# Performance work log

Hardware: AMD Instinct MI355X
Metric: run time of the kernel (lower is better)

The kernel has to match this reference:

```python
import jax, jax.numpy as jnp
import numpy as np

N = 20000
M = 32          # max_neighbors
IN_DIM = 256
OUT_DIM = 256
H = 4           # num_heads
D = OUT_DIM // H  # head_dim = 64
LN_EPS = 1e-5
NEG_INF = -1.0e9


def setup_inputs() -> dict:
    key = jax.random.key(0)
    ks = jax.random.split(key, 6)
    h = jax.random.normal(ks[0], (N, IN_DIM), dtype=jnp.float32)
    neighbor_idx = jax.random.randint(ks[1], (N, M), 0, N, dtype=jnp.int32)
    neighbor_mask = jax.random.randint(ks[2], (N, M), 0, 2, dtype=jnp.int32)
    # parameters (xavier-ish scaling)
    W = jax.random.normal(ks[3], (IN_DIM, OUT_DIM), dtype=jnp.float32) / np.sqrt(IN_DIM)
    a_l = jax.random.normal(ks[4], (H, D), dtype=jnp.float32) / np.sqrt(D)
    a_r = jax.random.normal(ks[5], (H, D), dtype=jnp.float32) / np.sqrt(D)
    ln_gamma = jnp.ones((OUT_DIM,), dtype=jnp.float32)
    ln_beta = jnp.zeros((OUT_DIM,), dtype=jnp.float32)
    return {"h": h, "neighbor_idx": neighbor_idx, "neighbor_mask": neighbor_mask,
            "W": W, "a_l": a_l, "a_r": a_r, "ln_gamma": ln_gamma, "ln_beta": ln_beta}


def reference(h, neighbor_idx, neighbor_mask, W, a_l, a_r, ln_gamma, ln_beta):
    h_proj = h @ W                                   # [N, OUT_DIM]
    h_heads = h_proj.reshape(N, H, D)                # [N, H, D]
    # per-node score halves; gathering scalars instead of full features for er
    el = jnp.einsum('nhd,hd->nh', h_heads, a_l)      # [N, H]
    er_node = jnp.einsum('nhd,hd->nh', h_heads, a_r) # [N, H]
    er = er_node[neighbor_idx]                       # [N, M, H]
    e = jax.nn.leaky_relu(el[:, None, :] + er, negative_slope=0.2)  # [N, M, H]
    e = jnp.where(neighbor_mask[:, :, None] == 0, NEG_INF, e)
    alpha = jax.nn.softmax(e, axis=1)                # softmax over neighbors
    neigh_h = h_heads[neighbor_idx]                  # [N, M, H, D]
    out_heads = jnp.einsum('nmh,nmhd->nhd', alpha, neigh_h)
    H_cat = out_heads.reshape(N, OUT_DIM)
    res = h_proj                                     # in_dim == out_dim -> res_proj is None
    out = jax.nn.gelu(H_cat + res, approximate=False)
    # LayerNorm over last dim
    mu = jnp.mean(out, axis=-1, keepdims=True)
    var = jnp.var(out, axis=-1, keepdims=True)
    out = (out - mu) * jax.lax.rsqrt(var + LN_EPS) * ln_gamma + ln_beta
    return out
```

## Files before the change

kernel.cpp:

```cpp
#include <hip/hip_runtime.h>
#include <math.h>

#define N_NODES 20000
#define M_NEI   32
#define DIM     256
#define H_HEADS 4
#define D_HEAD  64
#define LN_EPS  1e-5f
#define NEG_INF -1.0e9f
#define APAD    264

using short8  = __attribute__((ext_vector_type(8))) short;
using short4v = __attribute__((ext_vector_type(4))) short;
using floatx4 = __attribute__((ext_vector_type(4))) float;
using floatx2 = __attribute__((ext_vector_type(2))) float;
using uintx4  = __attribute__((ext_vector_type(4))) unsigned int;

__device__ __forceinline__ float bf2f(unsigned short u) {
    union { unsigned int i; float f; } c; c.i = ((unsigned int)u) << 16; return c.f;
}
__device__ __forceinline__ float u2f(unsigned int i) {
    union { unsigned int i; float f; } c; c.i = i; return c.f;
}
__device__ __forceinline__ unsigned short f2bf(float f) {
    union { float f; unsigned int i; } c; c.f = f;
    unsigned int x = c.i;
    x += 0x7fffu + ((x >> 16) & 1u);
    return (unsigned short)(x >> 16);
}
__device__ __forceinline__ bool in_is_fp32(const void* gamma) {
    return *(const unsigned int*)gamma == 0x3F800000u;
}

__global__ void k_prep(const void* __restrict__ W, const void* __restrict__ gamma,
                       unsigned short* __restrict__ Wt) {
    const bool f32 = in_is_fp32(gamma);
    const int n = blockIdx.x;
    const int k = threadIdx.x;
    float w = f32 ? ((const float*)W)[(size_t)k * DIM + n]
                  : bf2f(((const unsigned short*)W)[(size_t)k * DIM + n]);
    Wt[(size_t)n * DIM + k] = f2bf(w);
}

__global__ __launch_bounds__(256) void k_gemm(const void* __restrict__ A,
                                              const void* __restrict__ gamma,
                                              const unsigned short* __restrict__ Bt,
                                              const void* __restrict__ al,
                                              const void* __restrict__ ar,
                                              unsigned short* __restrict__ hp_h,
                                              float* __restrict__ el_h,
                                              float* __restrict__ er_h) {
    __shared__ unsigned short sA[32][APAD];
    const bool f32 = in_is_fp32(gamma);
    const int t    = threadIdx.x;
    const int m0   = blockIdx.x * 32;

    #pragma unroll
    for (int it = 0; it < 4; ++it) {
        int chunk = it * 256 + t;
        int row   = chunk >> 5;
        int c16   = chunk & 31;
        short8 v;
        if (!f32) {
            v = *(const short8*)((const unsigned short*)A + (size_t)(m0 + row) * DIM + c16 * 8);
        } else {
            const float* ap = (const float*)A + (size_t)(m0 + row) * DIM + c16 * 8;
            #pragma unroll
            for (int j = 0; j < 8; ++j) v[j] = (short)f2bf(ap[j]);
        }
        *(short8*)&sA[row][c16 * 8] = v;
    }
    __syncthreads();

    const int hd   = t >> 6;
    const int lane = t & 63;
    const int r    = lane & 15;
    const int quad = lane >> 4;
    const int n0   = hd * 64;

    floatx4 acc[2][4];
    #pragma unroll
    for (int rf = 0; rf < 2; ++rf)
        #pragma unroll
        for (int c = 0; c < 4; ++c) acc[rf][c] = (floatx4){0.f, 0.f, 0.f, 0.f};

    #pragma unroll
    for (int k0 = 0; k0 < DIM; k0 += 32) {
        short8 a0 = *(const short8*)&sA[r][k0 + quad * 8];
        short8 a1 = *(const short8*)&sA[16 + r][k0 + quad * 8];
        #pragma unroll
        for (int c = 0; c < 4; ++c) {
            short8 b = *(const short8*)(Bt + (size_t)(n0 + c * 16 + r) * DIM + k0 + quad * 8);
            acc[0][c] = __builtin_amdgcn_mfma_f32_16x16x32_bf16(a0, b, acc[0][c], 0, 0, 0);
            acc[1][c] = __builtin_amdgcn_mfma_f32_16x16x32_bf16(a1, b, acc[1][c], 0, 0, 0);
        }
    }

    float alv[4], arv[4];
    #pragma unroll
    for (int c = 0; c < 4; ++c) {
        int col = n0 + c * 16 + r;
        if (f32) { alv[c] = ((const float*)al)[col]; arv[c] = ((const float*)ar)[col]; }
        else     { alv[c] = bf2f(((const unsigned short*)al)[col]);
                   arv[c] = bf2f(((const unsigned short*)ar)[col]); }
    }

    #pragma unroll
    for (int rf = 0; rf < 2; ++rf) {
        #pragma unroll
        for (int rr = 0; rr < 4; ++rr) {
            const int row = m0 + rf * 16 + quad * 4 + rr;
            float sl = 0.f, sr = 0.f;
            #pragma unroll
            for (int c = 0; c < 4; ++c) {
                float v = acc[rf][c][rr];
                sl += v * alv[c];
                sr += v * arv[c];
                hp_h[((size_t)hd * N_NODES + row) * D_HEAD + c * 16 + r] = f2bf(v);
            }
            #pragma unroll
            for (int off = 1; off < 16; off <<= 1) {
                sl += __shfl_xor(sl, off);
                sr += __shfl_xor(sr, off);
            }
            if (r == 0) {
                el_h[(size_t)hd * N_NODES + row] = sl;
                er_h[(size_t)hd * N_NODES + row] = sr;
            }
        }
    }
}

__global__ __launch_bounds__(256) void k_attn_h(const int* __restrict__ nidx,
                                                const int* __restrict__ nmask,
                                                const unsigned short* __restrict__ hp_h,
                                                const float* __restrict__ el_h,
                                                const float* __restrict__ er_h,
                                                unsigned short* __restrict__ out_h) {
    __shared__ int2 s_oa[32][33];

    const int hd  = blockIdx.x & 3;
    const int nb0 = (blockIdx.x >> 2) * 32;
    const int t   = threadIdx.x;

    {
        const int m   = t & 31;
        const int sub = t >> 5;
        #pragma unroll
        for (int it = 0; it < 4; ++it) {
            const int nl  = it * 8 + sub;
            const int n   = nb0 + nl;
            const int idx = nidx[(size_t)n * M_NEI + m];
            const int msk = nmask[(size_t)n * M_NEI + m];
            float e = el_h[(size_t)hd * N_NODES + n] + er_h[(size_t)hd * N_NODES + idx];
            e = (e > 0.f) ? e : 0.2f * e;
            e = msk ? e : NEG_INF;
            float mx = e;
            #pragma unroll
            for (int off = 1; off < 32; off <<= 1) mx = fmaxf(mx, __shfl_xor(mx, off, 32));
            float a = expf(e - mx);
            float sm = a;
            #pragma unroll
            for (int off = 1; off < 32; off <<= 1) sm += __shfl_xor(sm, off, 32);
            int2 oa;
            oa.x = idx * (D_HEAD * 2);
            union { float f; int i; } c; c.f = a / sm;
            oa.y = c.i;
            s_oa[nl][m] = oa;
        }
    }
    __syncthreads();

    const int wave = t >> 6;
    const int lane = t & 63;
    const int g    = lane >> 3;
    const int s    = lane & 7;
    const int nl   = wave * 8 + g;
    const int n    = nb0 + nl;
    const char* tbl = (const char*)hp_h + (size_t)hd * N_NODES * (D_HEAD * 2) + s * 16;

    floatx2 acc[4];
    #pragma unroll
    for (int j = 0; j < 4; ++j) acc[j] = (floatx2){0.f, 0.f};

    #pragma unroll
    for (int m = 0; m < M_NEI; ++m) {
        const int2  oa = s_oa[nl][m];
        const float aa = u2f((unsigned int)oa.y);
        uintx4 u = *(const uintx4*)(tbl + oa.x);
        #pragma unroll
        for (int j = 0; j < 4; ++j) {
            floatx2 f = { u2f(u[j] << 16), u2f(u[j] & 0xffff0000u) };
            acc[j] += (floatx2){aa, aa} * f;
        }
    }

    {
        uintx4 u = *(const uintx4*)((const char*)hp_h
                     + ((size_t)hd * N_NODES + n) * (D_HEAD * 2) + s * 16);
        #pragma unroll
        for (int j = 0; j < 4; ++j) {
            floatx2 f = { u2f(u[j] << 16), u2f(u[j] & 0xffff0000u) };
            acc[j] += f;
        }
    }

    short8 o;
    #pragma unroll
    for (int j = 0; j < 4; ++j) {
        o[2 * j]     = (short)f2bf(acc[j][0]);
        o[2 * j + 1] = (short)f2bf(acc[j][1]);
    }
    *(short8*)(out_h + ((size_t)hd * N_NODES + n) * D_HEAD + s * 8) = o;
}

__global__ __launch_bounds__(256) void k_final(const unsigned short* __restrict__ out_h,
                                               const void* __restrict__ gamma,
                                               const void* __restrict__ beta,
                                               void* __restrict__ out) {
    const bool f32 = in_is_fp32(gamma);
    const int wave = threadIdx.x >> 6;
    const int lane = threadIdx.x & 63;
    const int n    = blockIdx.x * 4 + wave;
    const int h    = lane >> 4;
    const int d0   = (lane & 15) * 4;

    const size_t off = ((size_t)h * N_NODES + n) * D_HEAD + d0;
    short4v ov = *(const short4v*)(out_h + off);

    float x[4], s1 = 0.f, s2 = 0.f;
    #pragma unroll
    for (int i = 0; i < 4; ++i) {
        float xi = bf2f((unsigned short)ov[i]);
        xi = 0.5f * xi * (1.f + erff(xi * 0.70710678118654752f));
        x[i] = xi;
        s1 += xi;
        s2 += xi * xi;
    }
    #pragma unroll
    for (int offv = 1; offv < 64; offv <<= 1) {
        s1 += __shfl_xor(s1, offv);
        s2 += __shfl_xor(s2, offv);
    }
    const float mu  = s1 * (1.f / 256.f);
    float var = s2 * (1.f / 256.f) - mu * mu;
    var = fmaxf(var, 0.f);
    const float inv = rsqrtf(var + LN_EPS);

    if (f32) {
        const float* gp = (const float*)gamma + lane * 4;
        const float* bp = (const float*)beta  + lane * 4;
        float* op = (float*)out + (size_t)n * DIM + lane * 4;
        #pragma unroll
        for (int i = 0; i < 4; ++i)
            op[i] = (x[i] - mu) * inv * gp[i] + bp[i];
    } else {
        const unsigned short* gp = (const unsigned short*)gamma + lane * 4;
        const unsigned short* bp = (const unsigned short*)beta  + lane * 4;
        short4v o;
        #pragma unroll
        for (int i = 0; i < 4; ++i) {
            float y = (x[i] - mu) * inv * bf2f(gp[i]) + bf2f(bp[i]);
            o[i] = (short)f2bf(y);
        }
        *(short4v*)((unsigned short*)out + (size_t)n * DIM + lane * 4) = o;
    }
}

extern "C" void kernel_launch(void* const* d_in, const int* in_sizes, int n_in,
                              void* d_out, int out_size, void* d_ws, size_t ws_size,
                              hipStream_t stream) {
    const void* h     = d_in[0];
    const int*  nidx  = (const int*)d_in[1];
    const int*  nmask = (const int*)d_in[2];
    const void* W     = d_in[3];
    const void* al    = d_in[4];
    const void* ar    = d_in[5];
    const void* gamma = d_in[6];
    const void* beta  = d_in[7];

    unsigned short* Wt    = (unsigned short*)d_ws;
    unsigned short* hp_h  = (unsigned short*)((char*)d_ws + 131072);
    unsigned short* out_h = (unsigned short*)((char*)d_ws + 10371072);
    float* el_h = (float*)((char*)d_ws + 20611072);
    float* er_h = (float*)((char*)d_ws + 20931072);

    k_prep<<<DIM, 256, 0, stream>>>(W, gamma, Wt);
    k_gemm<<<N_NODES / 32, 256, 0, stream>>>(h, gamma, Wt, al, ar, hp_h, el_h, er_h);
    k_attn_h<<<H_HEADS * (N_NODES / 32), 256, 0, stream>>>(nidx, nmask, hp_h, el_h, er_h, out_h);
    k_final<<<N_NODES / 4, 256, 0, stream>>>(out_h, gamma, beta, d_out);
}
```

Baseline: 135.9 us.

## Compact masked neighbors, use fast exp/erf, vectorize loads and stores

The attention kernel now ballots the neighbor mask and compacts only the valid neighbors into shared memory with their softmax weights, then gathers features for just those entries. This roughly halves the gather traffic when about half the mask is zero. Several smaller changes ride along: the softmax uses exp2 and a reciprocal instead of expf and a divide, GELU uses a polynomial erf approximation, the fp32 input loads in the GEMM and the LayerNorm output stores are vectorized, and the GEMM gets a launch-bounds occupancy hint. The trade-offs are some loss of accuracy in erf and exp, an extra zero-fill pass with a sync, and a variable-length loop in place of a fully unrolled one.

```diff
diff --git a/kernel.cpp b/kernel.cpp
--- a/kernel.cpp
+++ b/kernel.cpp
@@ -15,6 +15,7 @@
 using floatx4 = __attribute__((ext_vector_type(4))) float;
 using floatx2 = __attribute__((ext_vector_type(2))) float;
 using uintx4  = __attribute__((ext_vector_type(4))) unsigned int;
+using uintx2  = __attribute__((ext_vector_type(2))) unsigned int;
 
 __device__ __forceinline__ float bf2f(unsigned short u) {
     union { unsigned int i; float f; } c; c.i = ((unsigned int)u) << 16; return c.f;
@@ -30,6 +31,21 @@
 }
 __device__ __forceinline__ bool in_is_fp32(const void* gamma) {
     return *(const unsigned int*)gamma == 0x3F800000u;
+}
+__device__ __forceinline__ float fast_exp(float x) {
+    return __builtin_amdgcn_exp2f(x * 1.44269504088896341f);
+}
+__device__ __forceinline__ float erf_fast(float x) {
+    float ax = fabsf(x);
+    float t  = __builtin_amdgcn_rcpf(fmaf(0.3275911f, ax, 1.0f));
+    float p  = fmaf(1.061405429f, t, -1.453152027f);
+    p = fmaf(p, t, 1.421413741f);
+    p = fmaf(p, t, -0.284496736f);
+    p = fmaf(p, t, 0.254829592f);
+    p = p * t;
+    float e  = __builtin_amdgcn_exp2f(-ax * ax * 1.44269504088896341f);
+    float r  = fmaf(-p, e, 1.0f);
+    return copysignf(r, x);
 }
 
 __global__ void k_prep(const void* __restrict__ W, const void* __restrict__ gamma,
@@ -42,18 +58,23 @@
     Wt[(size_t)n * DIM + k] = f2bf(w);
 }
 
-__global__ __launch_bounds__(256) void k_gemm(const void* __restrict__ A,
-                                              const void* __restrict__ gamma,
-                                              const unsigned short* __restrict__ Bt,
-                                              const void* __restrict__ al,
-                                              const void* __restrict__ ar,
-                                              unsigned short* __restrict__ hp_h,
-                                              float* __restrict__ el_h,
-                                              float* __restrict__ er_h) {
+__global__ __launch_bounds__(256, 2) void k_gemm(const void* __restrict__ A,
+                                                 const void* __restrict__ gamma,
+                                                 const unsigned short* __restrict__ Bt,
+                                                 const void* __restrict__ al,
+                                                 const void* __restrict__ ar,
+                                                 unsigned short* __restrict__ hp_h,
+                                                 float* __restrict__ el_h,
+                                                 float* __restrict__ er_h) {
     __shared__ unsigned short sA[32][APAD];
     const bool f32 = in_is_fp32(gamma);
     const int t    = threadIdx.x;
     const int m0   = blockIdx.x * 32;
+    const int hd   = t >> 6;
+    const int lane = t & 63;
+    const int r    = lane & 15;
+    const int quad = lane >> 4;
+    const int n0   = hd * 64;
 
     #pragma unroll
     for (int it = 0; it < 4; ++it) {
@@ -65,18 +86,17 @@
             v = *(const short8*)((const unsigned short*)A + (size_t)(m0 + row) * DIM + c16 * 8);
         } else {
             const float* ap = (const float*)A + (size_t)(m0 + row) * DIM + c16 * 8;
-            #pragma unroll
-            for (int j = 0; j < 8; ++j) v[j] = (short)f2bf(ap[j]);
+            floatx4 f0 = *(const floatx4*)ap;
+            floatx4 f1 = *(const floatx4*)(ap + 4);
+            #pragma unroll
+            for (int j = 0; j < 4; ++j) {
+                v[j]     = (short)f2bf(f0[j]);
+                v[4 + j] = (short)f2bf(f1[j]);
+            }
         }
         *(short8*)&sA[row][c16 * 8] = v;
     }
     __syncthreads();
-
-    const int hd   = t >> 6;
-    const int lane = t & 63;
-    const int r    = lane & 15;
-    const int quad = lane >> 4;
-    const int n0   = hd * 64;
 
     floatx4 acc[2][4];
     #pragma unroll
@@ -131,17 +151,24 @@
     }
 }
 
-__global__ __launch_bounds__(256) void k_attn_h(const int* __restrict__ nidx,
-                                                const int* __restrict__ nmask,
-                                                const unsigned short* __restrict__ hp_h,
-                                                const float* __restrict__ el_h,
-                                                const float* __restrict__ er_h,
-                                                unsigned short* __restrict__ out_h) {
+__global__ __launch_bounds__(256) void k_attn(const int* __restrict__ nidx,
+                                              const int* __restrict__ nmask,
+                                              const unsigned short* __restrict__ hp_h,
+                                              const float* __restrict__ el_h,
+                                              const float* __restrict__ er_h,
+                                              unsigned short* __restrict__ out_h) {
     __shared__ int2 s_oa[32][33];
+    __shared__ int  s_cnt[32];
 
     const int hd  = blockIdx.x & 3;
     const int nb0 = (blockIdx.x >> 2) * 32;
     const int t   = threadIdx.x;
+
+    {
+        int2* p = &s_oa[0][0];
+        for (int i = t; i < 32 * 33; i += 256) p[i] = (int2){0, 0};
+    }
+    __syncthreads();
 
     {
         const int m   = t & 31;
@@ -158,15 +185,27 @@
             float mx = e;
             #pragma unroll
             for (int off = 1; off < 32; off <<= 1) mx = fmaxf(mx, __shfl_xor(mx, off, 32));
-            float a = expf(e - mx);
+            float a = fast_exp(e - mx);
             float sm = a;
             #pragma unroll
             for (int off = 1; off < 32; off <<= 1) sm += __shfl_xor(sm, off, 32);
-            int2 oa;
-            oa.x = idx * (D_HEAD * 2);
-            union { float f; int i; } c; c.f = a / sm;
-            oa.y = c.i;
-            s_oa[nl][m] = oa;
+            a *= __builtin_amdgcn_rcpf(sm);
+
+            unsigned long long bal64 = __ballot(msk != 0);
+            unsigned int bal = (t & 32) ? (unsigned int)(bal64 >> 32)
+                                        : (unsigned int)bal64;
+            int  cnt   = __popc(bal);
+            bool valid = (msk != 0);
+            if (cnt == 0) { valid = true; cnt = 32; bal = 0xffffffffu; }
+            if (valid) {
+                int pfx = __popc(bal & ((1u << m) - 1u));
+                int2 oa;
+                oa.x = idx * (D_HEAD * 2);
+                union { float f; int i; } c; c.f = a;
+                oa.y = c.i;
+                s_oa[nl][pfx] = oa;
+            }
+            if (m == 0) s_cnt[nl] = cnt;
         }
     }
     __syncthreads();
@@ -177,21 +216,24 @@
     const int s    = lane & 7;
     const int nl   = wave * 8 + g;
     const int n    = nb0 + nl;
+    const int cnt  = s_cnt[nl];
     const char* tbl = (const char*)hp_h + (size_t)hd * N_NODES * (D_HEAD * 2) + s * 16;
 
     floatx2 acc[4];
     #pragma unroll
     for (int j = 0; j < 4; ++j) acc[j] = (floatx2){0.f, 0.f};
 
-    #pragma unroll
-    for (int m = 0; m < M_NEI; ++m) {
-        const int2  oa = s_oa[nl][m];
-        const float aa = u2f((unsigned int)oa.y);
-        uintx4 u = *(const uintx4*)(tbl + oa.x);
-        #pragma unroll
-        for (int j = 0; j < 4; ++j) {
-            floatx2 f = { u2f(u[j] << 16), u2f(u[j] & 0xffff0000u) };
-            acc[j] += (floatx2){aa, aa} * f;
+    for (int m = 0; m < cnt; m += 4) {
+        #pragma unroll
+        for (int k = 0; k < 4; ++k) {
+            const int2  oa = s_oa[nl][m + k];
+            const float aa = u2f((unsigned int)oa.y);
+            uintx4 u = *(const uintx4*)(tbl + oa.x);
+            #pragma unroll
+            for (int j = 0; j < 4; ++j) {
+                floatx2 f = { u2f(u[j] << 16), u2f(u[j] & 0xffff0000u) };
+                acc[j] += (floatx2){aa, aa} * f;
+            }
         }
     }
 
@@ -232,7 +274,7 @@
     #pragma unroll
     for (int i = 0; i < 4; ++i) {
         float xi = bf2f((unsigned short)ov[i]);
-        xi = 0.5f * xi * (1.f + erff(xi * 0.70710678118654752f));
+        xi = 0.5f * xi * (1.f + erf_fast(xi * 0.70710678118654752f));
         x[i] = xi;
         s1 += xi;
         s2 += xi * xi;
@@ -250,10 +292,11 @@
     if (f32) {
         const float* gp = (const float*)gamma + lane * 4;
         const float* bp = (const float*)beta  + lane * 4;
-        float* op = (float*)out + (size_t)n * DIM + lane * 4;
+        floatx4 o;
         #pragma unroll
         for (int i = 0; i < 4; ++i)
-            op[i] = (x[i] - mu) * inv * gp[i] + bp[i];
+            o[i] = (x[i] - mu) * inv * gp[i] + bp[i];
+        *(floatx4*)((float*)out + (size_t)n * DIM + lane * 4) = o;
     } else {
         const unsigned short* gp = (const unsigned short*)gamma + lane * 4;
         const unsigned short* bp = (const unsigned short*)beta  + lane * 4;
@@ -279,14 +322,14 @@
     const void* gamma = d_in[6];
     const void* beta  = d_in[7];
 
-    unsigned short* Wt    = (unsigned short*)d_ws;
-    unsigned short* hp_h  = (unsigned short*)((char*)d_ws + 131072);
-    unsigned short* out_h = (unsigned short*)((char*)d_ws + 10371072);
-    float* el_h = (float*)((char*)d_ws + 20611072);
-    float* er_h = (float*)((char*)d_ws + 20931072);
-
-    k_prep<<<DIM, 256, 0, stream>>>(W, gamma, Wt);
-    k_gemm<<<N_NODES / 32, 256, 0, stream>>>(h, gamma, Wt, al, ar, hp_h, el_h, er_h);
-    k_attn_h<<<H_HEADS * (N_NODES / 32), 256, 0, stream>>>(nidx, nmask, hp_h, el_h, er_h, out_h);
+    unsigned short* hp_h  = (unsigned short*)d_ws;
+    unsigned short* out_h = (unsigned short*)((char*)d_ws + 10240000);
+    float* el_h = (float*)((char*)d_ws + 20480000);
+    float* er_h = (float*)((char*)d_ws + 20800000);
+    unsigned short* Wt = (unsigned short*)((char*)d_ws + 21120000);
+
+    k_prep <<<DIM, 256, 0, stream>>>(W, gamma, Wt);
+    k_gemm <<<N_NODES / 32, 256, 0, stream>>>(h, gamma, Wt, al, ar, hp_h, el_h, er_h);
+    k_attn <<<H_HEADS * (N_NODES / 32), 256, 0, stream>>>(nidx, nmask, hp_h, el_h, er_h, out_h);
     k_final<<<N_NODES / 4, 256, 0, stream>>>(out_h, gamma, beta, d_out);
 }
```

Measured after the change: 131.7 us. -3.1%, faster.
